# Kernel tuning notes

Measured on AMD Instinct MI355X. Metric: run time of the kernel, lower is better.

## Reference

```python
import jax, jax.numpy as jnp
import numpy as np

GAMMAS = (0.001, 0.01, 0.1, 1.0, 10.0, 100.0, 1000.0)
EPS = 1e-30


def setup_inputs() -> dict:
    key = jax.random.key(0)
    k1, k2 = jax.random.split(key)
    x = jax.random.normal(k1, (8192, 128), dtype=jnp.float32)
    y = jax.random.normal(k2, (8192, 128), dtype=jnp.float32)
    return {"x": x, "y": y}


def _cdist_sq(x1, x2):
    # squared Euclidean distance matrix, clamped at 1e-30 (matches my_cdist)
    x1_norm = jnp.sum(x1 * x1, axis=-1, keepdims=True)          # [N,1]
    x2_norm = jnp.sum(x2 * x2, axis=-1, keepdims=True)          # [M,1]
    d = x1_norm + x2_norm.T - 2.0 * (x1 @ x2.T)                 # [N,M]
    return jnp.maximum(d, EPS)


def _gaussian_kernel_mean(x, y):
    d = _cdist_sq(x, y)
    # sum over 7 bandwidths, fused into one pass conceptually
    k = sum(jnp.exp(d * (-g)) for g in GAMMAS)
    return jnp.mean(k)


def reference(x, y):
    kxx = _gaussian_kernel_mean(x, x)
    kyy = _gaussian_kernel_mean(y, y)
    kxy = _gaussian_kernel_mean(x, y)
    return kxx + kyy - 2.0 * kxy
```

## Files before the change

kernel.cpp:

```cpp
#include <hip/hip_runtime.h>


#define N_PTS 8192
#define D 128
#define TILES 64
#define TRI 2080
#define NBLK (2 * TRI + TILES * TILES)

typedef __attribute__((ext_vector_type(8))) short bf16x8;
typedef __attribute__((ext_vector_type(8))) unsigned short u16x8;
typedef __attribute__((ext_vector_type(4))) float f32x4;

__device__ __forceinline__ unsigned short f2bf(float a) {
  unsigned u = __float_as_uint(a);
  return (unsigned short)((u + 0x7FFFu + ((u >> 16) & 1u)) >> 16);
}
__device__ __forceinline__ float bf2f(unsigned short b) {
  return __uint_as_float(((unsigned)b) << 16);
}

__global__ __launch_bounds__(256) void norms_kernel(const float* __restrict__ x,
                                                    const float* __restrict__ y,
                                                    float* __restrict__ nx,
                                                    float* __restrict__ ny) {
  int tid = threadIdx.x;
  int g = tid & 3;
  int row = ((int)blockIdx.x & 127) * 64 + (tid >> 2);
  int arr = (int)blockIdx.x >> 7;
  const float* src = arr ? y : x;
  const float4* p = (const float4*)(src + (size_t)row * D) + g;
  float s = 0.f;
  #pragma unroll
  for (int i = 0; i < 8; i++) {
    float4 v = p[i * 4];
    s += v.x * v.x + v.y * v.y + v.z * v.z + v.w * v.w;
  }
  s += __shfl_xor(s, 1);
  s += __shfl_xor(s, 2);
  if (g == 0) (arr ? ny : nx)[row] = s;
}

__global__ __launch_bounds__(256) void convert_kernel(const float* __restrict__ x,
                                                      const float* __restrict__ y,
                                                      unsigned short* __restrict__ xf,
                                                      unsigned short* __restrict__ yf) {
  __shared__ float lds[4][16][132];
  int tid = threadIdx.x;
  int lane = tid & 63, wv = tid >> 6;
  int grp = (int)blockIdx.x * 4 + wv;
  int arr = grp >> 9;
  int rowgrp = grp & 511;
  const float* src = (arr ? y : x) + (size_t)rowgrp * 16 * D;
  unsigned short* dst = (arr ? yf : xf) + (size_t)rowgrp * 4096;

  #pragma unroll
  for (int it = 0; it < 8; it++) {
    int slot = it * 64 + lane;
    int row = slot >> 5, f4 = slot & 31;
    float4 v = *(const float4*)(src + row * D + f4 * 4);
    *(float4*)&lds[wv][row][f4 * 4] = v;
  }
  __syncthreads();

  int row = lane & 15, koct = lane >> 4;
  #pragma unroll
  for (int ks = 0; ks < 8; ks++) {
    int kp = ks * 32 + koct * 8;
    int kf = kp & 127;
    bool ishi = kp < 128;
    float v[8];
    *(float4*)&v[0] = *(const float4*)&lds[wv][row][kf];
    *(float4*)&v[4] = *(const float4*)&lds[wv][row][kf + 4];
    u16x8 o;
    #pragma unroll
    for (int j = 0; j < 8; j++) {
      unsigned short h = f2bf(v[j]);
      o[j] = ishi ? h : f2bf(v[j] - bf2f(h));
    }
    *(u16x8*)(dst + ks * 512 + lane * 8) = o;
  }
}

__global__ __launch_bounds__(256) void mmd_tile128_kernel(
    const unsigned short* __restrict__ xf, const unsigned short* __restrict__ yf,
    const float* __restrict__ nx, const float* __restrict__ ny,
    double* __restrict__ acc_out) {
  __shared__ unsigned short As[2][4096];
  __shared__ unsigned short Bs[2][4096];
  __shared__ double red[4];

  int bid = blockIdx.x;
  const unsigned short *Af, *Bf;
  const float *nA, *nB;
  float w;
  int ib, jb;
  bool isdiag = false;
  if (bid < 2 * TRI) {
    int t = (bid < TRI) ? bid : bid - TRI;
    int r = 0;
    while (t >= TILES - r) { t -= TILES - r; r++; }
    ib = r; jb = r + t;
    if (bid < TRI) { Af = xf; Bf = xf; nA = nx; nB = nx; }
    else           { Af = yf; Bf = yf; nA = ny; nB = ny; }
    isdiag = (ib == jb);
    w = isdiag ? 1.0f : 2.0f;
  } else {
    int t = bid - 2 * TRI;
    ib = t >> 6; jb = t & 63;
    Af = xf; Bf = yf; nA = nx; nB = ny;
    w = -2.0f;
  }

  int tid = threadIdx.x;
  int lane = tid & 63, wv = tid >> 6;
  int wm = wv >> 1, wn = wv & 1;
  int r16 = lane & 15, g4 = lane >> 4;

  const unsigned short* Afrag = Af + (size_t)(ib * 8) * 4096;
  const unsigned short* Bfrag = Bf + (size_t)(jb * 8) * 4096;

  #define STAGE(ks, buf)                                                        \
    {                                                                           \
      _Pragma("unroll")                                                         \
      for (int i = 0; i < 4; i++) {                                             \
        int s = wv * 4 + i;                                                     \
        const unsigned short* g = (s < 8)                                       \
            ? (Afrag + (size_t)s * 4096 + (ks) * 512 + lane * 8)                \
            : (Bfrag + (size_t)(s - 8) * 4096 + (ks) * 512 + lane * 8);         \
        unsigned short* l = (s < 8) ? &As[buf][s * 512] : &Bs[buf][(s - 8) * 512]; \
        __builtin_amdgcn_global_load_lds(                                       \
            (const __attribute__((address_space(1))) void*)g,                   \
            (__attribute__((address_space(3))) void*)l, 16, 0, 0);              \
      }                                                                         \
    }

  f32x4 acc[4][4];
  #pragma unroll
  for (int m = 0; m < 4; m++)
    #pragma unroll
    for (int n = 0; n < 4; n++) acc[m][n] = (f32x4){0.f, 0.f, 0.f, 0.f};

  STAGE(0, 0);
  __syncthreads();

  #pragma unroll
  for (int ks = 0; ks < 8; ks++) {
    int cur = ks & 1;
    if (ks < 7) STAGE(ks + 1, cur ^ 1);
    bf16x8 a[4], b[4];
    #pragma unroll
    for (int m = 0; m < 4; m++)
      a[m] = *(const bf16x8*)&As[cur][(wm * 4 + m) * 512 + lane * 8];
    #pragma unroll
    for (int n = 0; n < 4; n++)
      b[n] = *(const bf16x8*)&Bs[cur][(wn * 4 + n) * 512 + lane * 8];
    #pragma unroll
    for (int m = 0; m < 4; m++)
      #pragma unroll
      for (int n = 0; n < 4; n++)
        acc[m][n] = __builtin_amdgcn_mfma_f32_16x16x32_bf16(a[m], b[n], acc[m][n], 0, 0, 0);
    __syncthreads();
  }

  const float* nArow = nA + ib * 128;
  const float* nBrow = nB + jb * 128;
  float nb4[4];
  #pragma unroll
  for (int n = 0; n < 4; n++) nb4[n] = nBrow[wn * 64 + n * 16 + r16];

  float lsum = 0.f;
  #pragma unroll
  for (int m = 0; m < 4; m++) {
    float na4[4];
    #pragma unroll
    for (int r = 0; r < 4; r++) na4[r] = nArow[wm * 64 + m * 16 + g4 * 4 + r];
    float dv[4][4];
    float dmin = 3.0e38f;
    #pragma unroll
    for (int n = 0; n < 4; n++) {
      #pragma unroll
      for (int r = 0; r < 4; r++) {
        float dd = fmaf(-2.f, acc[m][n][r], na4[r] + nb4[n]);
        dd = fmaxf(dd, 1e-30f);
        int rl = wm * 64 + m * 16 + g4 * 4 + r;
        int cl = wn * 64 + n * 16 + r16;
        if (isdiag && rl == cl) dd = 1e30f;
        dv[n][r] = dd;
        dmin = fminf(dmin, dd);
      }
    }
    if (__all(dmin > 110.f)) {
      #pragma unroll
      for (int n = 0; n < 4; n++)
        #pragma unroll
        for (int r = 0; r < 4; r++) {
          float dd = dv[n][r];
          lsum += __expf(dd * -0.001f);
          lsum += __expf(dd * -0.01f);
          lsum += __expf(dd * -0.1f);
        }
    } else {
      #pragma unroll
      for (int n = 0; n < 4; n++)
        #pragma unroll
        for (int r = 0; r < 4; r++) {
          float dd = dv[n][r];
          lsum += __expf(dd * -0.001f);
          lsum += __expf(dd * -0.01f);
          lsum += __expf(dd * -0.1f);
          lsum += __expf(dd * -1.0f);
          lsum += __expf(dd * -10.0f);
          lsum += __expf(dd * -100.0f);
          lsum += __expf(dd * -1000.0f);
        }
    }
  }

  double v = (double)lsum * (double)w;
  v += __shfl_xor(v, 32);
  v += __shfl_xor(v, 16);
  v += __shfl_xor(v, 8);
  v += __shfl_xor(v, 4);
  v += __shfl_xor(v, 2);
  v += __shfl_xor(v, 1);
  if (lane == 0) red[wv] = v;
  __syncthreads();
  if (tid == 0) {
    double s = red[0] + red[1] + red[2] + red[3];
    atomicAdd(acc_out, s);
  }
  #undef STAGE
}

__global__ __launch_bounds__(256) void mmd_fallback_kernel(const float* __restrict__ X,
                                                           const float* __restrict__ Y,
                                                           const float* __restrict__ nx,
                                                           const float* __restrict__ ny,
                                                           double* __restrict__ acc_out) {
  __shared__ unsigned short As[128 * 64];
  __shared__ unsigned short Bs[128 * 64];
  __shared__ double red[256];
  int bid = blockIdx.x;
  const float *A, *B, *nA, *nB;
  float w;
  int ib, jb;
  bool isdiag = false;
  if (bid < 2 * TRI) {
    int t = (bid < TRI) ? bid : bid - TRI;
    int r = 0;
    while (t >= TILES - r) { t -= TILES - r; r++; }
    ib = r; jb = r + t;
    if (bid < TRI) { A = X; B = X; nA = nx; nB = nx; }
    else           { A = Y; B = Y; nA = ny; nB = ny; }
    isdiag = (ib == jb);
    w = isdiag ? 1.0f : 2.0f;
  } else {
    int t = bid - 2 * TRI;
    ib = t >> 6; jb = t & 63;
    A = X; B = Y; nA = nx; nB = ny;
    w = -2.0f;
  }
  int tid = threadIdx.x;
  int lane = tid & 63;
  int wv = tid >> 6, wm = wv >> 1, wn = wv & 1;
  int r16 = lane & 15, g4 = lane >> 4;
  const float* Ab = A + (size_t)ib * 128 * D;
  const float* Bb = B + (size_t)jb * 128 * D;
  f32x4 acc[4][4];
  #pragma unroll
  for (int m = 0; m < 4; m++)
    #pragma unroll
    for (int n = 0; n < 4; n++) acc[m][n] = (f32x4){0.f, 0.f, 0.f, 0.f};
  #pragma unroll 1
  for (int kc = 0; kc < 4; kc++) {
    int k0f = (kc & 1) * 64;
    bool ishi = (kc < 2);
    __syncthreads();
    #pragma unroll
    for (int s = 0; s < 4; s++) {
      int slot = tid + s * 256;
      int row = slot >> 3;
      int k2 = (slot & 7) * 8;
      const float* pa = Ab + row * D + k0f + k2;
      const float* pb = Bb + row * D + k0f + k2;
      float4 a0 = *(const float4*)pa;
      float4 a1 = *(const float4*)(pa + 4);
      float4 b0 = *(const float4*)pb;
      float4 b1 = *(const float4*)(pb + 4);
      float av[8] = {a0.x, a0.y, a0.z, a0.w, a1.x, a1.y, a1.z, a1.w};
      float bv[8] = {b0.x, b0.y, b0.z, b0.w, b1.x, b1.y, b1.z, b1.w};
      u16x8 ua, ub;
      #pragma unroll
      for (int j = 0; j < 8; j++) {
        unsigned short ha = f2bf(av[j]);
        unsigned short hb = f2bf(bv[j]);
        if (ishi) { ua[j] = (short)ha; ub[j] = (short)hb; }
        else {
          ua[j] = f2bf(av[j] - bf2f(ha));
          ub[j] = f2bf(bv[j] - bf2f(hb));
        }
      }
      int boff = row * 128 + ((k2 * 2) ^ ((row & 7) << 4));
      *(u16x8*)((char*)As + boff) = ua;
      *(u16x8*)((char*)Bs + boff) = ub;
    }
    __syncthreads();
    #pragma unroll
    for (int ks = 0; ks < 2; ks++) {
      bf16x8 af[4], bfr[4];
      int kb = ks * 64 + g4 * 16;
      #pragma unroll
      for (int m = 0; m < 4; m++) {
        int row = wm * 64 + m * 16 + r16;
        af[m] = *(const bf16x8*)((const char*)As + row * 128 + (kb ^ ((row & 7) << 4)));
      }
      #pragma unroll
      for (int n = 0; n < 4; n++) {
        int row = wn * 64 + n * 16 + r16;
        bfr[n] = *(const bf16x8*)((const char*)Bs + row * 128 + (kb ^ ((row & 7) << 4)));
      }
      #pragma unroll
      for (int m = 0; m < 4; m++)
        #pragma unroll
        for (int n = 0; n < 4; n++)
          acc[m][n] = __builtin_amdgcn_mfma_f32_16x16x32_bf16(af[m], bfr[n], acc[m][n], 0, 0, 0);
    }
  }
  const float* nArow = nA + ib * 128;
  const float* nBrow = nB + jb * 128;
  float nb4[4];
  #pragma unroll
  for (int n = 0; n < 4; n++) nb4[n] = nBrow[wn * 64 + n * 16 + r16];
  float lsum = 0.f;
  #pragma unroll
  for (int m = 0; m < 4; m++) {
    float na4[4];
    #pragma unroll
    for (int r = 0; r < 4; r++) na4[r] = nArow[wm * 64 + m * 16 + g4 * 4 + r];
    float dv[4][4];
    float dmin = 3.0e38f;
    #pragma unroll
    for (int n = 0; n < 4; n++) {
      #pragma unroll
      for (int r = 0; r < 4; r++) {
        float dd = fmaf(-2.f, acc[m][n][r], na4[r] + nb4[n]);
        dd = fmaxf(dd, 1e-30f);
        int rl = wm * 64 + m * 16 + g4 * 4 + r;
        int cl = wn * 64 + n * 16 + r16;
        if (isdiag && rl == cl) dd = 1e30f;
        dv[n][r] = dd;
        dmin = fminf(dmin, dd);
      }
    }
    if (__all(dmin > 110.f)) {
      #pragma unroll
      for (int n = 0; n < 4; n++)
        #pragma unroll
        for (int r = 0; r < 4; r++) {
          float dd = dv[n][r];
          lsum += __expf(dd * -0.001f);
          lsum += __expf(dd * -0.01f);
          lsum += __expf(dd * -0.1f);
        }
    } else {
      #pragma unroll
      for (int n = 0; n < 4; n++)
        #pragma unroll
        for (int r = 0; r < 4; r++) {
          float dd = dv[n][r];
          lsum += __expf(dd * -0.001f);
          lsum += __expf(dd * -0.01f);
          lsum += __expf(dd * -0.1f);
          lsum += __expf(dd * -1.0f);
          lsum += __expf(dd * -10.0f);
          lsum += __expf(dd * -100.0f);
          lsum += __expf(dd * -1000.0f);
        }
    }
  }
  red[tid] = (double)lsum * (double)w;
  __syncthreads();
  #pragma unroll
  for (int s = 128; s > 0; s >>= 1) {
    if (tid < s) red[tid] += red[tid + s];
    __syncthreads();
  }
  if (tid == 0) atomicAdd(acc_out, red[0]);
}

__global__ __launch_bounds__(256) void diag_kernel(const float* __restrict__ x,
                                                   const float* __restrict__ y,
                                                   const float* __restrict__ nx,
                                                   const float* __restrict__ ny,
                                                   double* __restrict__ acc_out) {
  __shared__ double red[256];
  int tid = threadIdx.x;
  int idx = (int)blockIdx.x * 256 + tid;
  int arr = idx >> 13;
  int row = idx & 8191;
  const float* src = (arr ? y : x) + (size_t)row * D;
  float n = (arr ? ny : nx)[row];
  float acc = 0.f;
  #pragma unroll 4
  for (int k4 = 0; k4 < 32; k4++) {
    float4 v = *(const float4*)(src + k4 * 4);
    acc = fmaf(v.x, v.x, acc);
    acc = fmaf(v.y, v.y, acc);
    acc = fmaf(v.z, v.z, acc);
    acc = fmaf(v.w, v.w, acc);
  }
  float d = fmaf(-2.f, acc, n + n);
  d = fmaxf(d, 1e-30f);
  float s = 0.f;
  s += __expf(d * -0.001f);
  s += __expf(d * -0.01f);
  s += __expf(d * -0.1f);
  s += __expf(d * -1.0f);
  s += __expf(d * -10.0f);
  s += __expf(d * -100.0f);
  s += __expf(d * -1000.0f);
  red[tid] = (double)s;
  __syncthreads();
  #pragma unroll
  for (int st = 128; st > 0; st >>= 1) {
    if (tid < st) red[tid] += red[tid + st];
    __syncthreads();
  }
  if (tid == 0) atomicAdd(acc_out, red[0]);
}

__global__ void finalize_kernel(const double* __restrict__ acc,
                                float* __restrict__ out) {
  out[0] = (float)(acc[0] * (1.0 / ((double)N_PTS * (double)N_PTS)));
}

extern "C" void kernel_launch(void* const* d_in, const int* in_sizes, int n_in,
                              void* d_out, int out_size, void* d_ws, size_t ws_size,
                              hipStream_t stream) {
  const float* x = (const float*)d_in[0];
  const float* y = (const float*)d_in[1];
  float* out = (float*)d_out;

  char* ws = (char*)d_ws;
  double* acc = (double*)ws;
  float* nx = (float*)(ws + 4096);
  float* ny = (float*)(ws + 36864);
  const size_t FRAG_OFF = 69632;
  const size_t FRAG_SZ = 4194304;
  const size_t NEED = FRAG_OFF + 2 * FRAG_SZ;

  hipMemsetAsync(acc, 0, sizeof(double), stream);
  hipLaunchKernelGGL(norms_kernel, dim3(256), dim3(256), 0, stream, x, y, nx, ny);
  if (ws_size >= NEED) {
    unsigned short* xf = (unsigned short*)(ws + FRAG_OFF);
    unsigned short* yf = (unsigned short*)(ws + FRAG_OFF + FRAG_SZ);
    hipLaunchKernelGGL(convert_kernel, dim3(256), dim3(256), 0, stream, x, y, xf, yf);
    hipLaunchKernelGGL(mmd_tile128_kernel, dim3(NBLK), dim3(256), 0, stream,
                       xf, yf, nx, ny, acc);
  } else {
    hipLaunchKernelGGL(mmd_fallback_kernel, dim3(NBLK), dim3(256), 0, stream, x, y, nx, ny, acc);
  }
  hipLaunchKernelGGL(diag_kernel, dim3(64), dim3(256), 0, stream, x, y, nx, ny, acc);
  hipLaunchKernelGGL(finalize_kernel, dim3(1), dim3(1), 0, stream, acc, out);
}
```

Before: 210.2 us.

## Fuse norms into convert, diag into MMD kernel, triple-buffer K loop

Computes row norms inside the bf16 conversion kernel from data already staged in LDS, removing the separate norms launch. The diagonal-correction work is folded into the tile kernel as extra blocks, removing another launch. The K loop moves to a three-buffer LDS pipeline with explicit vmcnt waits and a single barrier per step, and the epilogue is specialised so off-diagonal tiles skip the diagonal check. These cut launch overhead and per-step synchronisation at the cost of more LDS per block, which may lower occupancy.

```diff
diff --git a/kernel.cpp b/kernel.cpp
--- a/kernel.cpp
+++ b/kernel.cpp
@@ -6,6 +6,7 @@
 #define TILES 64
 #define TRI 2080
 #define NBLK (2 * TRI + TILES * TILES)
+#define NDIAG 64
 
 typedef __attribute__((ext_vector_type(8))) short bf16x8;
 typedef __attribute__((ext_vector_type(8))) unsigned short u16x8;
@@ -19,31 +20,12 @@
   return __uint_as_float(((unsigned)b) << 16);
 }
 
-__global__ __launch_bounds__(256) void norms_kernel(const float* __restrict__ x,
-                                                    const float* __restrict__ y,
-                                                    float* __restrict__ nx,
-                                                    float* __restrict__ ny) {
-  int tid = threadIdx.x;
-  int g = tid & 3;
-  int row = ((int)blockIdx.x & 127) * 64 + (tid >> 2);
-  int arr = (int)blockIdx.x >> 7;
-  const float* src = arr ? y : x;
-  const float4* p = (const float4*)(src + (size_t)row * D) + g;
-  float s = 0.f;
-  #pragma unroll
-  for (int i = 0; i < 8; i++) {
-    float4 v = p[i * 4];
-    s += v.x * v.x + v.y * v.y + v.z * v.z + v.w * v.w;
-  }
-  s += __shfl_xor(s, 1);
-  s += __shfl_xor(s, 2);
-  if (g == 0) (arr ? ny : nx)[row] = s;
-}
-
 __global__ __launch_bounds__(256) void convert_kernel(const float* __restrict__ x,
                                                       const float* __restrict__ y,
                                                       unsigned short* __restrict__ xf,
-                                                      unsigned short* __restrict__ yf) {
+                                                      unsigned short* __restrict__ yf,
+                                                      float* __restrict__ nx,
+                                                      float* __restrict__ ny) {
   __shared__ float lds[4][16][132];
   int tid = threadIdx.x;
   int lane = tid & 63, wv = tid >> 6;
@@ -52,6 +34,7 @@
   int rowgrp = grp & 511;
   const float* src = (arr ? y : x) + (size_t)rowgrp * 16 * D;
   unsigned short* dst = (arr ? yf : xf) + (size_t)rowgrp * 4096;
+  float* nrm = (arr ? ny : nx) + rowgrp * 16;
 
   #pragma unroll
   for (int it = 0; it < 8; it++) {
@@ -61,6 +44,19 @@
     *(float4*)&lds[wv][row][f4 * 4] = v;
   }
   __syncthreads();
+
+  {
+    int row = lane >> 2, q = lane & 3;
+    float s = 0.f;
+    #pragma unroll
+    for (int i = 0; i < 8; i++) {
+      float4 v = *(const float4*)&lds[wv][row][q * 4 + i * 16];
+      s += v.x * v.x + v.y * v.y + v.z * v.z + v.w * v.w;
+    }
+    s += __shfl_xor(s, 1);
+    s += __shfl_xor(s, 2);
+    if (q == 0) nrm[row] = s;
+  }
 
   int row = lane & 15, koct = lane >> 4;
   #pragma unroll
@@ -83,13 +79,53 @@
 
 __global__ __launch_bounds__(256) void mmd_tile128_kernel(
     const unsigned short* __restrict__ xf, const unsigned short* __restrict__ yf,
+    const float* __restrict__ x, const float* __restrict__ y,
     const float* __restrict__ nx, const float* __restrict__ ny,
     double* __restrict__ acc_out) {
-  __shared__ unsigned short As[2][4096];
-  __shared__ unsigned short Bs[2][4096];
+  __shared__ unsigned short As[3][4096];
+  __shared__ unsigned short Bs[3][4096];
   __shared__ double red[4];
 
   int bid = blockIdx.x;
+  int tid = threadIdx.x;
+
+  if (bid >= NBLK) {
+    double* redd = (double*)As;
+    int idx = (bid - NBLK) * 256 + tid;
+    int arr = idx >> 13;
+    int row = idx & 8191;
+    const float* src = (arr ? y : x) + (size_t)row * D;
+    float n = (arr ? ny : nx)[row];
+    float acc = 0.f;
+    #pragma unroll 4
+    for (int k4 = 0; k4 < 32; k4++) {
+      float4 v = *(const float4*)(src + k4 * 4);
+      acc = fmaf(v.x, v.x, acc);
+      acc = fmaf(v.y, v.y, acc);
+      acc = fmaf(v.z, v.z, acc);
+      acc = fmaf(v.w, v.w, acc);
+    }
+    float d = fmaf(-2.f, acc, n + n);
+    d = fmaxf(d, 1e-30f);
+    float s = 0.f;
+    s += __expf(d * -0.001f);
+    s += __expf(d * -0.01f);
+    s += __expf(d * -0.1f);
+    s += __expf(d * -1.0f);
+    s += __expf(d * -10.0f);
+    s += __expf(d * -100.0f);
+    s += __expf(d * -1000.0f);
+    redd[tid] = (double)s;
+    __syncthreads();
+    #pragma unroll
+    for (int st = 128; st > 0; st >>= 1) {
+      if (tid < st) redd[tid] += redd[tid + st];
+      __syncthreads();
+    }
+    if (tid == 0) atomicAdd(acc_out, redd[0]);
+    return;
+  }
+
   const unsigned short *Af, *Bf;
   const float *nA, *nB;
   float w;
@@ -111,7 +147,6 @@
     w = -2.0f;
   }
 
-  int tid = threadIdx.x;
   int lane = tid & 63, wv = tid >> 6;
   int wm = wv >> 1, wn = wv & 1;
   int r16 = lane & 15, g4 = lane >> 4;
@@ -141,12 +176,18 @@
     for (int n = 0; n < 4; n++) acc[m][n] = (f32x4){0.f, 0.f, 0.f, 0.f};
 
   STAGE(0, 0);
-  __syncthreads();
 
   #pragma unroll
   for (int ks = 0; ks < 8; ks++) {
-    int cur = ks & 1;
-    if (ks < 7) STAGE(ks + 1, cur ^ 1);
+    int cur = ks % 3;
+    if (ks < 7) {
+      STAGE(ks + 1, (ks + 1) % 3);
+      asm volatile("s_waitcnt vmcnt(4)" ::: "memory");
+    } else {
+      asm volatile("s_waitcnt vmcnt(0)" ::: "memory");
+    }
+    __builtin_amdgcn_s_barrier();
+    __builtin_amdgcn_sched_barrier(0);
     bf16x8 a[4], b[4];
     #pragma unroll
     for (int m = 0; m < 4; m++)
@@ -159,7 +200,6 @@
       #pragma unroll
       for (int n = 0; n < 4; n++)
         acc[m][n] = __builtin_amdgcn_mfma_f32_16x16x32_bf16(a[m], b[n], acc[m][n], 0, 0, 0);
-    __syncthreads();
   }
 
   const float* nArow = nA + ib * 128;
@@ -169,52 +209,59 @@
   for (int n = 0; n < 4; n++) nb4[n] = nBrow[wn * 64 + n * 16 + r16];
 
   float lsum = 0.f;
-  #pragma unroll
-  for (int m = 0; m < 4; m++) {
-    float na4[4];
-    #pragma unroll
-    for (int r = 0; r < 4; r++) na4[r] = nArow[wm * 64 + m * 16 + g4 * 4 + r];
-    float dv[4][4];
-    float dmin = 3.0e38f;
-    #pragma unroll
-    for (int n = 0; n < 4; n++) {
-      #pragma unroll
-      for (int r = 0; r < 4; r++) {
-        float dd = fmaf(-2.f, acc[m][n][r], na4[r] + nb4[n]);
-        dd = fmaxf(dd, 1e-30f);
-        int rl = wm * 64 + m * 16 + g4 * 4 + r;
-        int cl = wn * 64 + n * 16 + r16;
-        if (isdiag && rl == cl) dd = 1e30f;
-        dv[n][r] = dd;
-        dmin = fminf(dmin, dd);
-      }
-    }
-    if (__all(dmin > 110.f)) {
-      #pragma unroll
-      for (int n = 0; n < 4; n++)
-        #pragma unroll
-        for (int r = 0; r < 4; r++) {
-          float dd = dv[n][r];
-          lsum += __expf(dd * -0.001f);
-          lsum += __expf(dd * -0.01f);
-          lsum += __expf(dd * -0.1f);
-        }
-    } else {
-      #pragma unroll
-      for (int n = 0; n < 4; n++)
-        #pragma unroll
-        for (int r = 0; r < 4; r++) {
-          float dd = dv[n][r];
-          lsum += __expf(dd * -0.001f);
-          lsum += __expf(dd * -0.01f);
-          lsum += __expf(dd * -0.1f);
-          lsum += __expf(dd * -1.0f);
-          lsum += __expf(dd * -10.0f);
-          lsum += __expf(dd * -100.0f);
-          lsum += __expf(dd * -1000.0f);
-        }
-    }
-  }
+  #define EPILOGUE(DIAGCHK)                                                     \
+    _Pragma("unroll")                                                           \
+    for (int m = 0; m < 4; m++) {                                               \
+      float na4[4];                                                             \
+      _Pragma("unroll")                                                         \
+      for (int r = 0; r < 4; r++) na4[r] = nArow[wm * 64 + m * 16 + g4 * 4 + r];\
+      float dv[4][4];                                                           \
+      float dmin = 3.0e38f;                                                     \
+      _Pragma("unroll")                                                         \
+      for (int n = 0; n < 4; n++) {                                             \
+        _Pragma("unroll")                                                       \
+        for (int r = 0; r < 4; r++) {                                           \
+          float dd = fmaf(-2.f, acc[m][n][r], na4[r] + nb4[n]);                 \
+          dd = fmaxf(dd, 1e-30f);                                               \
+          if (DIAGCHK) {                                                        \
+            int rl = wm * 64 + m * 16 + g4 * 4 + r;                             \
+            int cl = wn * 64 + n * 16 + r16;                                    \
+            if (rl == cl) dd = 1e30f;          \
+          }                                                                     \
+          dv[n][r] = dd;                                                        \
+          dmin = fminf(dmin, dd);                                               \
+        }                                                                       \
+      }                                                                         \
+      if (__all(dmin > 110.f)) {                                                \
+                   \
+        _Pragma("unroll")                                                       \
+        for (int n = 0; n < 4; n++)                                             \
+          _Pragma("unroll")                                                     \
+          for (int r = 0; r < 4; r++) {                                         \
+            float dd = dv[n][r];                                                \
+            lsum += __expf(dd * -0.001f);                                       \
+            lsum += __expf(dd * -0.01f);                                        \
+            lsum += __expf(dd * -0.1f);                                         \
+          }                                                                     \
+      } else {                                                                  \
+        _Pragma("unroll")                                                       \
+        for (int n = 0; n < 4; n++)                                             \
+          _Pragma("unroll")                                                     \
+          for (int r = 0; r < 4; r++) {                                         \
+            float dd = dv[n][r];                                                \
+            lsum += __expf(dd * -0.001f);                                       \
+            lsum += __expf(dd * -0.01f);                                        \
+            lsum += __expf(dd * -0.1f);                                         \
+            lsum += __expf(dd * -1.0f);                                         \
+            lsum += __expf(dd * -10.0f);                                        \
+            lsum += __expf(dd * -100.0f);                                       \
+            lsum += __expf(dd * -1000.0f);                                      \
+          }                                                                     \
+      }                                                                         \
+    }
+
+  if (isdiag) { EPILOGUE(true) } else { EPILOGUE(false) }
+  #undef EPILOGUE
 
   double v = (double)lsum * (double)w;
   v += __shfl_xor(v, 32);
@@ -429,6 +476,27 @@
   if (tid == 0) atomicAdd(acc_out, red[0]);
 }
 
+__global__ __launch_bounds__(256) void norms_kernel(const float* __restrict__ x,
+                                                    const float* __restrict__ y,
+                                                    float* __restrict__ nx,
+                                                    float* __restrict__ ny) {
+  int tid = threadIdx.x;
+  int g = tid & 3;
+  int row = ((int)blockIdx.x & 127) * 64 + (tid >> 2);
+  int arr = (int)blockIdx.x >> 7;
+  const float* src = arr ? y : x;
+  const float4* p = (const float4*)(src + (size_t)row * D) + g;
+  float s = 0.f;
+  #pragma unroll
+  for (int i = 0; i < 8; i++) {
+    float4 v = p[i * 4];
+    s += v.x * v.x + v.y * v.y + v.z * v.z + v.w * v.w;
+  }
+  s += __shfl_xor(s, 1);
+  s += __shfl_xor(s, 2);
+  if (g == 0) (arr ? ny : nx)[row] = s;
+}
+
 __global__ void finalize_kernel(const double* __restrict__ acc,
                                 float* __restrict__ out) {
   out[0] = (float)(acc[0] * (1.0 / ((double)N_PTS * (double)N_PTS)));
@@ -450,16 +518,17 @@
   const size_t NEED = FRAG_OFF + 2 * FRAG_SZ;
 
   hipMemsetAsync(acc, 0, sizeof(double), stream);
-  hipLaunchKernelGGL(norms_kernel, dim3(256), dim3(256), 0, stream, x, y, nx, ny);
   if (ws_size >= NEED) {
     unsigned short* xf = (unsigned short*)(ws + FRAG_OFF);
     unsigned short* yf = (unsigned short*)(ws + FRAG_OFF + FRAG_SZ);
-    hipLaunchKernelGGL(convert_kernel, dim3(256), dim3(256), 0, stream, x, y, xf, yf);
-    hipLaunchKernelGGL(mmd_tile128_kernel, dim3(NBLK), dim3(256), 0, stream,
-                       xf, yf, nx, ny, acc);
+    hipLaunchKernelGGL(convert_kernel, dim3(256), dim3(256), 0, stream,
+                       x, y, xf, yf, nx, ny);
+    hipLaunchKernelGGL(mmd_tile128_kernel, dim3(NBLK + NDIAG), dim3(256), 0, stream,
+                       xf, yf, x, y, nx, ny, acc);
   } else {
+    hipLaunchKernelGGL(norms_kernel, dim3(256), dim3(256), 0, stream, x, y, nx, ny);
     hipLaunchKernelGGL(mmd_fallback_kernel, dim3(NBLK), dim3(256), 0, stream, x, y, nx, ny, acc);
-  }
-  hipLaunchKernelGGL(diag_kernel, dim3(64), dim3(256), 0, stream, x, y, nx, ny, acc);
+    hipLaunchKernelGGL(diag_kernel, dim3(64), dim3(256), 0, stream, x, y, nx, ny, acc);
+  }
   hipLaunchKernelGGL(finalize_kernel, dim3(1), dim3(1), 0, stream, acc, out);
 }
```

Measured after the change: 217.0 us. 1.03x slower.
